# Optimization experiments

Hardware: AMD Instinct MI355X
Metric: run time of the kernel (lower is better)

## Reference

```python
import jax, jax.numpy as jnp
import numpy as np

K, M, NUM_HOM = 32, 16, 2
B, N = 32, 2048
EPS = 1e-12


def _safe_norm(x):
    # stable L2 norm over last axis, keepdims
    return jnp.sqrt(jnp.sum(x * x, axis=-1, keepdims=True) + EPS)


def setup_inputs() -> dict:
    key = jax.random.key(0)
    k1, k2, k3, k4, k5 = jax.random.split(key, 5)
    pts = jax.random.normal(k1, (B, N, M), jnp.float32)
    hom = jax.random.randint(k2, (B, N), 0, NUM_HOM).astype(jnp.float32)
    dgm = jnp.concatenate([hom[..., None], pts], axis=-1)  # [B,N,M+1]
    # ragged diagrams: zero-pad a suffix per batch element; the original
    # while-loop stops at the first all-zero row (count_nonzero == 0)
    lengths = jax.random.randint(k3, (B,), N // 2, N + 1)
    mask = (jnp.arange(N)[None, :] < lengths[:, None]).astype(jnp.float32)
    dgm = dgm * mask[..., None]
    theta = 0.05 * jax.random.normal(k4, (K, M), jnp.float32)
    class_w = 0.05 * jax.random.normal(k5, (NUM_HOM,), jnp.float32)
    return {"dgm": dgm, "theta": theta, "class_w": class_w}


def reference(dgm, theta, class_w):
    # dgm: [B,N,M+1]; col 0 = homology class, cols 1: = embedded point
    hom = dgm[..., 0].astype(jnp.int32)  # [B,N]
    y = dgm[..., 1:]                      # [B,N,M]
    # while-loop validity: hom <= 1 AND row not all-zero; early exit -> prefix mask
    valid_pt = (hom <= 1) & jnp.any(dgm != 0, axis=-1)
    valid = jnp.cumprod(valid_pt.astype(dgm.dtype), axis=1)  # [B,N]
    w = class_w[jnp.clip(hom, 0, class_w.shape[0] - 1)] * valid  # [B,N]
    # Poincare parametrization: scale by theta_k, map R^m -> ball (hyperboloid chart)
    u = y[:, :, None, :] * theta[None, None, :, :]  # [B,N,K,M]
    un = _safe_norm(u)
    x = u / (1.0 + jnp.sqrt(1.0 + un * un))         # ||x|| < 1
    # log map at origin x_o = 0, c = 1: atanh(||x||) * x/||x||
    xn = _safe_norm(x)
    t = jnp.arctanh(jnp.clip(xn, 0.0, 1.0 - 1e-5)) * x / xn  # [B,N,K,M]
    # weighted segment sum over points; note: `sum` in the original is NOT
    # reset between k iterations -> cumulative sum over bases k
    S = jnp.einsum('bn,bnkm->bkm', w, t)
    S = jnp.cumsum(S, axis=1)  # [B,K,M]
    # exp map at origin (c=1): tanh(||v||) * v/||v||
    Sn = _safe_norm(S)
    xd = jnp.tanh(Sn) * S / Sn
    # chart back to R^m (inverse of the ball parametrization)
    xdn2 = jnp.sum(xd * xd, axis=-1, keepdims=True)
    yd = 2.0 * xd / jnp.maximum(1.0 - xdn2, 1e-7)
    return yd.reshape(dgm.shape[0], K * M)
```

## Files before the change

### kernel.cpp

```cpp
#include <hip/hip_runtime.h>
#include <math.h>

#define B_ 32
#define N_ 2048
#define M_ 16
#define K_ 32
#define EPS 1e-12f

constexpr int NC      = 128;
constexpr int NCHUNK  = N_ / NC;
constexpr int THREADS = 256;
constexpr int YSTRIDE = 20;

__device__ __forceinline__ float fast_atanh(float x) {
    float ratio = (1.0f + x) * __builtin_amdgcn_rcpf(1.0f - x);
    return 0.34657359f * __log2f(ratio);
}

__global__ __launch_bounds__(THREADS) void pml_main_kernel(
    const float* __restrict__ dgm, const float* __restrict__ theta,
    const float* __restrict__ class_w,
    float* __restrict__ G_part, unsigned* __restrict__ finv_loc)
{
    __shared__ __align__(16) float y_lds[NC * YSTRIDE];
    __shared__ float hom_lds[NC];
    __shared__ float w_lds[NC];
    __shared__ unsigned wred[2];
    __shared__ float red[4][K_ * (M_ + 1)];

    const int b    = blockIdx.y;
    const int c    = blockIdx.x;
    const int tid  = threadIdx.x;
    const int k    = tid & (K_ - 1);
    const int grp  = tid >> 5;
    const int lane = tid & 63;
    const int wv   = tid >> 6;

    const float4* src4 = (const float4*)(dgm + ((size_t)b * N_ + c * NC) * (M_ + 1));
    for (int i4 = tid; i4 < NC * (M_ + 1) / 4; i4 += THREADS) {
        float4 v = src4[i4];
        int i  = i4 * 4;
        int nl = i / (M_ + 1);
        int j  = i - nl * (M_ + 1);
        float vv[4] = { v.x, v.y, v.z, v.w };
#pragma unroll
        for (int e = 0; e < 4; ++e) {
            if (j == 0) hom_lds[nl] = vv[e];
            else        y_lds[nl * YSTRIDE + (j - 1)] = vv[e];
            if (++j == M_ + 1) { j = 0; ++nl; }
        }
    }
    __syncthreads();

    const float cw0 = class_w[0], cw1 = class_w[1];
    if (tid < NC) {
        const float4* yv = (const float4*)(y_lds + tid * YSTRIDE);
        float4 a0 = yv[0], a1 = yv[1], a2 = yv[2], a3 = yv[3];
        float  h  = hom_lds[tid];
        bool nz = (h != 0.0f) |
                  (a0.x != 0.0f) | (a0.y != 0.0f) | (a0.z != 0.0f) | (a0.w != 0.0f) |
                  (a1.x != 0.0f) | (a1.y != 0.0f) | (a1.z != 0.0f) | (a1.w != 0.0f) |
                  (a2.x != 0.0f) | (a2.y != 0.0f) | (a2.z != 0.0f) | (a2.w != 0.0f) |
                  (a3.x != 0.0f) | (a3.y != 0.0f) | (a3.z != 0.0f) | (a3.w != 0.0f);
        bool ok = ((int)h <= 1) && nz;
        unsigned long long bal = __ballot(!ok);
        if (lane == 0)
            wred[wv] = bal ? (unsigned)(wv * 64 + (__ffsll((long long)bal) - 1))
                           : 0xFFFFFFFFu;
        int hc = min(max((int)h, 0), 1);
        w_lds[tid] = hc ? cw1 : cw0;
    }
    __syncthreads();
    const int local_mn = (int)min(min(wred[0], wred[1]), (unsigned)NC);

    float t2[M_];
#pragma unroll
    for (int m = 0; m < M_; ++m) { float t = theta[k * M_ + m]; t2[m] = t * t; }
    float g[M_];
#pragma unroll
    for (int m = 0; m < M_; ++m) g[m] = 0.0f;

    for (int nl = grp; nl < local_mn; nl += 8) {
        float w = w_lds[nl];
        const float4* yv = (const float4*)(y_lds + nl * YSTRIDE);
        float4 a0 = yv[0], a1 = yv[1], a2 = yv[2], a3 = yv[3];
        float y[M_] = { a0.x, a0.y, a0.z, a0.w,  a1.x, a1.y, a1.z, a1.w,
                        a2.x, a2.y, a2.z, a2.w,  a3.x, a3.y, a3.z, a3.w };
        float s = 0.0f;
#pragma unroll
        for (int m = 0; m < M_; ++m) s = fmaf(y[m] * y[m], t2[m], s);
        float d   = 1.0f + sqrtf(1.0f + s + EPS);
        float rd  = __builtin_amdgcn_rcpf(d);
        float xn2 = fmaf(s, rd * rd, EPS);
        float xn  = sqrtf(xn2);
        float inv_xnd = __builtin_amdgcn_rsqf(xn2) * rd;
        float xc  = fminf(xn, 1.0f - 1e-5f);
        float wc  = w * (fast_atanh(xc) * inv_xnd);
#pragma unroll
        for (int m = 0; m < M_; ++m) g[m] = fmaf(wc, y[m], g[m]);
    }

#pragma unroll
    for (int m = 0; m < M_; ++m) g[m] += __shfl_down(g[m], 32, 64);
    if (lane < K_) {
#pragma unroll
        for (int m = 0; m < M_; ++m) red[wv][lane * (M_ + 1) + m] = g[m];
    }
    __syncthreads();

    float* dst = G_part + (((size_t)b * NCHUNK + c) * K_ * M_);
    for (int p = tid; p < K_ * M_; p += THREADS) {
        int kk = p >> 4, m = p & 15;
        int idx = kk * (M_ + 1) + m;
        dst[p] = red[0][idx] + red[1][idx] + red[2][idx] + red[3][idx];
    }
    if (tid == 0) finv_loc[b * NCHUNK + c] = (unsigned)local_mn;
}

__global__ __launch_bounds__(256) void pml_epilogue_kernel(
    const float* __restrict__ G_part, const unsigned* __restrict__ finv_loc,
    const float* __restrict__ theta, float* __restrict__ out)
{
    __shared__ float S_lds[K_ * M_];
    __shared__ unsigned fl[NCHUNK];

    const int b   = blockIdx.x;
    const int tid = threadIdx.x;

    if (tid < NCHUNK) fl[tid] = finv_loc[b * NCHUNK + tid];
    __syncthreads();

    int ninc = NCHUNK;
    for (int cc = 0; cc < NCHUNK; ++cc) {
        if (fl[cc] < (unsigned)NC) { ninc = cc + 1; break; }
    }

    const float* Gb = G_part + (size_t)b * NCHUNK * K_ * M_;
    for (int e = tid; e < K_ * M_; e += 256) {
        float s = 0.0f;
        for (int cc = 0; cc < ninc; ++cc) s += Gb[cc * (K_ * M_) + e];
        S_lds[e] = s;
    }
    __syncthreads();

    if (tid < K_) {
        const int lane = tid;
        float S[M_];
#pragma unroll
        for (int m = 0; m < M_; ++m)
            S[m] = theta[lane * M_ + m] * S_lds[lane * M_ + m];

#pragma unroll
        for (int m = 0; m < M_; ++m) {
            float v = S[m];
#pragma unroll
            for (int off = 1; off < K_; off <<= 1) {
                float up = __shfl_up(v, off, 32);
                if (lane >= off) v += up;
            }
            S[m] = v;
        }

        float sn2 = 0.0f;
#pragma unroll
        for (int m = 0; m < M_; ++m) sn2 = fmaf(S[m], S[m], sn2);
        float Sn = sqrtf(sn2 + EPS);
        float e2 = __expf(-2.0f * Sn);
        float r  = (1.0f - e2) * __builtin_amdgcn_rcpf((1.0f + e2) * Sn);

        float xd[M_];
        float xdn2 = 0.0f;
#pragma unroll
        for (int m = 0; m < M_; ++m) { xd[m] = r * S[m]; xdn2 = fmaf(xd[m], xd[m], xdn2); }
        float scale = 2.0f / fmaxf(1.0f - xdn2, 1e-7f);

#pragma unroll
        for (int m = 0; m < M_; ++m)
            out[(size_t)b * (K_ * M_) + lane * M_ + m] = scale * xd[m];
    }
}

extern "C" void kernel_launch(void* const* d_in, const int* in_sizes, int n_in,
                              void* d_out, int out_size, void* d_ws, size_t ws_size,
                              hipStream_t stream) {
    const float* dgm     = (const float*)d_in[0];
    const float* theta   = (const float*)d_in[1];
    const float* class_w = (const float*)d_in[2];
    float* out = (float*)d_out;

    float*    G_part   = (float*)d_ws;
    unsigned* finv_loc = (unsigned*)((char*)d_ws +
                         (size_t)B_ * NCHUNK * K_ * M_ * sizeof(float));

    dim3 grid(NCHUNK, B_);
    pml_main_kernel<<<grid, THREADS, 0, stream>>>(dgm, theta, class_w, G_part, finv_loc);

    pml_epilogue_kernel<<<B_, 256, 0, stream>>>(G_part, finv_loc, theta, out);
}
```

Measured before the change: 75.76 us.

## Fuse main and epilogue into single per-batch kernel with double-buffered chunk streaming

Replaces the chunk-parallel main kernel plus epilogue with one kernel per batch element of 1024 threads that streams chunks sequentially through double-buffered LDS, prefetching the next chunk while computing the current one. It exits early once an invalid row is found, skipping padded data, and reduces partial sums in LDS before applying the cumulative scan and exp/chart map. This removes the second launch and the global partial-sum round trip, but cuts the grid to 32 blocks and serialises chunk processing within each block.

```diff
diff --git a/kernel.cpp b/kernel.cpp
--- a/kernel.cpp
+++ b/kernel.cpp
@@ -9,95 +9,113 @@
 
 constexpr int NC      = 128;
 constexpr int NCHUNK  = N_ / NC;
-constexpr int THREADS = 256;
+constexpr int TPB     = 1024;
+constexpr int NWAVE   = TPB / 64;
 constexpr int YSTRIDE = 20;
+constexpr int F4      = NC * (M_ + 1) / 4;
 
 __device__ __forceinline__ float fast_atanh(float x) {
     float ratio = (1.0f + x) * __builtin_amdgcn_rcpf(1.0f - x);
     return 0.34657359f * __log2f(ratio);
 }
 
-__global__ __launch_bounds__(THREADS) void pml_main_kernel(
+__global__ __launch_bounds__(TPB) void pml_onepass_kernel(
     const float* __restrict__ dgm, const float* __restrict__ theta,
-    const float* __restrict__ class_w,
-    float* __restrict__ G_part, unsigned* __restrict__ finv_loc)
+    const float* __restrict__ class_w, float* __restrict__ out)
 {
-    __shared__ __align__(16) float y_lds[NC * YSTRIDE];
-    __shared__ float hom_lds[NC];
+    __shared__ __align__(16) float y_lds[2][NC * YSTRIDE];
+    __shared__ float hom_lds[2][NC];
     __shared__ float w_lds[NC];
     __shared__ unsigned wred[2];
-    __shared__ float red[4][K_ * (M_ + 1)];
+    __shared__ float red[NWAVE][K_ * (M_ + 1)];
+    __shared__ float S_lds[K_ * M_];
 
-    const int b    = blockIdx.y;
-    const int c    = blockIdx.x;
+    const int b    = blockIdx.x;
     const int tid  = threadIdx.x;
     const int k    = tid & (K_ - 1);
     const int grp  = tid >> 5;
     const int lane = tid & 63;
     const int wv   = tid >> 6;
 
-    const float4* src4 = (const float4*)(dgm + ((size_t)b * N_ + c * NC) * (M_ + 1));
-    for (int i4 = tid; i4 < NC * (M_ + 1) / 4; i4 += THREADS) {
-        float4 v = src4[i4];
+    const float4* src4 = (const float4*)(dgm + (size_t)b * N_ * (M_ + 1));
+
+    auto scatter = [&](int p, float4 v, int i4) {
         int i  = i4 * 4;
         int nl = i / (M_ + 1);
         int j  = i - nl * (M_ + 1);
         float vv[4] = { v.x, v.y, v.z, v.w };
 #pragma unroll
         for (int e = 0; e < 4; ++e) {
-            if (j == 0) hom_lds[nl] = vv[e];
-            else        y_lds[nl * YSTRIDE + (j - 1)] = vv[e];
+            if (j == 0) hom_lds[p][nl] = vv[e];
+            else        y_lds[p][nl * YSTRIDE + (j - 1)] = vv[e];
             if (++j == M_ + 1) { j = 0; ++nl; }
         }
-    }
-    __syncthreads();
+    };
 
-    const float cw0 = class_w[0], cw1 = class_w[1];
-    if (tid < NC) {
-        const float4* yv = (const float4*)(y_lds + tid * YSTRIDE);
-        float4 a0 = yv[0], a1 = yv[1], a2 = yv[2], a3 = yv[3];
-        float  h  = hom_lds[tid];
-        bool nz = (h != 0.0f) |
-                  (a0.x != 0.0f) | (a0.y != 0.0f) | (a0.z != 0.0f) | (a0.w != 0.0f) |
-                  (a1.x != 0.0f) | (a1.y != 0.0f) | (a1.z != 0.0f) | (a1.w != 0.0f) |
-                  (a2.x != 0.0f) | (a2.y != 0.0f) | (a2.z != 0.0f) | (a2.w != 0.0f) |
-                  (a3.x != 0.0f) | (a3.y != 0.0f) | (a3.z != 0.0f) | (a3.w != 0.0f);
-        bool ok = ((int)h <= 1) && nz;
-        unsigned long long bal = __ballot(!ok);
-        if (lane == 0)
-            wred[wv] = bal ? (unsigned)(wv * 64 + (__ffsll((long long)bal) - 1))
-                           : 0xFFFFFFFFu;
-        int hc = min(max((int)h, 0), 1);
-        w_lds[tid] = hc ? cw1 : cw0;
-    }
-    __syncthreads();
-    const int local_mn = (int)min(min(wred[0], wred[1]), (unsigned)NC);
+    if (tid < F4) scatter(0, src4[tid], tid);
 
     float t2[M_];
 #pragma unroll
     for (int m = 0; m < M_; ++m) { float t = theta[k * M_ + m]; t2[m] = t * t; }
+    const float cw0 = class_w[0], cw1 = class_w[1];
+
     float g[M_];
 #pragma unroll
     for (int m = 0; m < M_; ++m) g[m] = 0.0f;
 
-    for (int nl = grp; nl < local_mn; nl += 8) {
-        float w = w_lds[nl];
-        const float4* yv = (const float4*)(y_lds + nl * YSTRIDE);
-        float4 a0 = yv[0], a1 = yv[1], a2 = yv[2], a3 = yv[3];
-        float y[M_] = { a0.x, a0.y, a0.z, a0.w,  a1.x, a1.y, a1.z, a1.w,
-                        a2.x, a2.y, a2.z, a2.w,  a3.x, a3.y, a3.z, a3.w };
-        float s = 0.0f;
+    __syncthreads();
+
+    int p = 0, c = 0;
+    for (;;) {
+        float4 vpre;
+        const bool have = (c + 1 < NCHUNK) && (tid < F4);
+        if (have) vpre = src4[(c + 1) * F4 + tid];
+
+        if (tid < NC) {
+            const float4* yv = (const float4*)(y_lds[p] + tid * YSTRIDE);
+            float4 a0 = yv[0], a1 = yv[1], a2 = yv[2], a3 = yv[3];
+            float  h  = hom_lds[p][tid];
+            bool nz = (h != 0.0f) |
+                      (a0.x != 0.0f) | (a0.y != 0.0f) | (a0.z != 0.0f) | (a0.w != 0.0f) |
+                      (a1.x != 0.0f) | (a1.y != 0.0f) | (a1.z != 0.0f) | (a1.w != 0.0f) |
+                      (a2.x != 0.0f) | (a2.y != 0.0f) | (a2.z != 0.0f) | (a2.w != 0.0f) |
+                      (a3.x != 0.0f) | (a3.y != 0.0f) | (a3.z != 0.0f) | (a3.w != 0.0f);
+            bool ok = ((int)h <= 1) && nz;
+            unsigned long long bal = __ballot(!ok);
+            if (lane == 0)
+                wred[wv] = bal ? (unsigned)(wv * 64 + (__ffsll((long long)bal) - 1))
+                               : 0xFFFFFFFFu;
+            int hc = min(max((int)h, 0), 1);
+            w_lds[tid] = hc ? cw1 : cw0;
+        }
+        __syncthreads();
+        const int local_mn = (int)min(min(wred[0], wred[1]), (unsigned)NC);
+
+        for (int nl = grp; nl < local_mn; nl += 32) {
+            float w = w_lds[nl];
+            const float4* yv = (const float4*)(y_lds[p] + nl * YSTRIDE);
+            float4 a0 = yv[0], a1 = yv[1], a2 = yv[2], a3 = yv[3];
+            float y[M_] = { a0.x, a0.y, a0.z, a0.w,  a1.x, a1.y, a1.z, a1.w,
+                            a2.x, a2.y, a2.z, a2.w,  a3.x, a3.y, a3.z, a3.w };
+            float s = 0.0f;
 #pragma unroll
-        for (int m = 0; m < M_; ++m) s = fmaf(y[m] * y[m], t2[m], s);
-        float d   = 1.0f + sqrtf(1.0f + s + EPS);
-        float rd  = __builtin_amdgcn_rcpf(d);
-        float xn2 = fmaf(s, rd * rd, EPS);
-        float xn  = sqrtf(xn2);
-        float inv_xnd = __builtin_amdgcn_rsqf(xn2) * rd;
-        float xc  = fminf(xn, 1.0f - 1e-5f);
-        float wc  = w * (fast_atanh(xc) * inv_xnd);
+            for (int m = 0; m < M_; ++m) s = fmaf(y[m] * y[m], t2[m], s);
+            float d   = 1.0f + sqrtf(1.0f + s + EPS);
+            float rd  = __builtin_amdgcn_rcpf(d);
+            float xn2 = fmaf(s, rd * rd, EPS);
+            float xn  = sqrtf(xn2);
+            float inv_xnd = __builtin_amdgcn_rsqf(xn2) * rd;
+            float xc  = fminf(xn, 1.0f - 1e-5f);
+            float wc  = w * (fast_atanh(xc) * inv_xnd);
 #pragma unroll
-        for (int m = 0; m < M_; ++m) g[m] = fmaf(wc, y[m], g[m]);
+            for (int m = 0; m < M_; ++m) g[m] = fmaf(wc, y[m], g[m]);
+        }
+
+        const bool done = (local_mn < NC) || (c + 1 == NCHUNK);
+        if (done) break;
+        if (have) scatter(p ^ 1, vpre, tid);
+        __syncthreads();
+        p ^= 1; ++c;
     }
 
 #pragma unroll
@@ -108,47 +126,21 @@
     }
     __syncthreads();
 
-    float* dst = G_part + (((size_t)b * NCHUNK + c) * K_ * M_);
-    for (int p = tid; p < K_ * M_; p += THREADS) {
-        int kk = p >> 4, m = p & 15;
-        int idx = kk * (M_ + 1) + m;
-        dst[p] = red[0][idx] + red[1][idx] + red[2][idx] + red[3][idx];
-    }
-    if (tid == 0) finv_loc[b * NCHUNK + c] = (unsigned)local_mn;
-}
-
-__global__ __launch_bounds__(256) void pml_epilogue_kernel(
-    const float* __restrict__ G_part, const unsigned* __restrict__ finv_loc,
-    const float* __restrict__ theta, float* __restrict__ out)
-{
-    __shared__ float S_lds[K_ * M_];
-    __shared__ unsigned fl[NCHUNK];
-
-    const int b   = blockIdx.x;
-    const int tid = threadIdx.x;
-
-    if (tid < NCHUNK) fl[tid] = finv_loc[b * NCHUNK + tid];
-    __syncthreads();
-
-    int ninc = NCHUNK;
-    for (int cc = 0; cc < NCHUNK; ++cc) {
-        if (fl[cc] < (unsigned)NC) { ninc = cc + 1; break; }
-    }
-
-    const float* Gb = G_part + (size_t)b * NCHUNK * K_ * M_;
-    for (int e = tid; e < K_ * M_; e += 256) {
+    for (int e = tid; e < K_ * M_; e += TPB) {
+        int kk = e >> 4, m = e & 15;
         float s = 0.0f;
-        for (int cc = 0; cc < ninc; ++cc) s += Gb[cc * (K_ * M_) + e];
+#pragma unroll
+        for (int w = 0; w < NWAVE; ++w) s += red[w][kk * (M_ + 1) + m];
         S_lds[e] = s;
     }
     __syncthreads();
 
     if (tid < K_) {
-        const int lane = tid;
+        const int klane = tid;
         float S[M_];
 #pragma unroll
         for (int m = 0; m < M_; ++m)
-            S[m] = theta[lane * M_ + m] * S_lds[lane * M_ + m];
+            S[m] = theta[klane * M_ + m] * S_lds[klane * M_ + m];
 
 #pragma unroll
         for (int m = 0; m < M_; ++m) {
@@ -156,7 +148,7 @@
 #pragma unroll
             for (int off = 1; off < K_; off <<= 1) {
                 float up = __shfl_up(v, off, 32);
-                if (lane >= off) v += up;
+                if (klane >= off) v += up;
             }
             S[m] = v;
         }
@@ -176,7 +168,7 @@
 
 #pragma unroll
         for (int m = 0; m < M_; ++m)
-            out[(size_t)b * (K_ * M_) + lane * M_ + m] = scale * xd[m];
+            out[(size_t)b * (K_ * M_) + klane * M_ + m] = scale * xd[m];
     }
 }
 
@@ -188,12 +180,5 @@
     const float* class_w = (const float*)d_in[2];
     float* out = (float*)d_out;
 
-    float*    G_part   = (float*)d_ws;
-    unsigned* finv_loc = (unsigned*)((char*)d_ws +
-                         (size_t)B_ * NCHUNK * K_ * M_ * sizeof(float));
-
-    dim3 grid(NCHUNK, B_);
-    pml_main_kernel<<<grid, THREADS, 0, stream>>>(dgm, theta, class_w, G_part, finv_loc);
-
-    pml_epilogue_kernel<<<B_, 256, 0, stream>>>(G_part, finv_loc, theta, out);
+    pml_onepass_kernel<<<B_, TPB, 0, stream>>>(dgm, theta, class_w, out);
 }
```

New measurement: 104.5 us. +37.9%, slower.
